# Optimization experiments

Measured on AMD Instinct MI355X. Metric: run time of the kernel, lower is better.

Reference implementation:

```python
import jax, jax.numpy as jnp
import numpy as np

D = 512
H = 8
W = 128  # window_size
HD = D // H
EPS = 1e-5


def _layernorm(x, g, b):
    mu = jnp.mean(x, axis=-1, keepdims=True)
    var = jnp.mean(jnp.square(x - mu), axis=-1, keepdims=True)
    return (x - mu) * jax.lax.rsqrt(var + EPS) * g + b


def setup_inputs() -> dict:
    key = jax.random.key(0)
    ks = jax.random.split(key, 6)
    B, S = 4, 8192
    src = jax.random.normal(ks[0], (B, S, D), jnp.float32)
    sc = 1.0 / np.sqrt(D)
    in_proj_w = jax.random.normal(ks[1], (3 * D, D), jnp.float32) * sc
    in_proj_b = jnp.zeros((3 * D,), jnp.float32)
    out_w = jax.random.normal(ks[2], (D, D), jnp.float32) * sc
    out_b = jnp.zeros((D,), jnp.float32)
    w1 = jax.random.normal(ks[3], (4 * D, D), jnp.float32) * sc
    b1 = jnp.zeros((4 * D,), jnp.float32)
    w2 = jax.random.normal(ks[4], (D, 4 * D), jnp.float32) * (1.0 / np.sqrt(4 * D))
    b2 = jnp.zeros((D,), jnp.float32)
    return {
        'src': src,
        'in_proj_w': in_proj_w, 'in_proj_b': in_proj_b,
        'out_w': out_w, 'out_b': out_b,
        'ln1_g': jnp.ones((D,), jnp.float32), 'ln1_b': jnp.zeros((D,), jnp.float32),
        'w1': w1, 'b1': b1, 'w2': w2, 'b2': b2,
        'ln2_g': jnp.ones((D,), jnp.float32), 'ln2_b': jnp.zeros((D,), jnp.float32),
    }


def reference(src, in_proj_w, in_proj_b, out_w, out_b, ln1_g, ln1_b,
              w1, b1, w2, b2, ln2_g, ln2_b):
    B, S, _ = src.shape
    nW = S // W
    x = src.reshape(B, nW, W, D)  # block-diagonal windows
    # packed qkv projection (torch MultiheadAttention in_proj)
    qkv = jnp.einsum('bnwd,ed->bnwe', x, in_proj_w) + in_proj_b
    q, k, v = jnp.split(qkv, 3, axis=-1)
    q = q.reshape(B, nW, W, H, HD)
    k = k.reshape(B, nW, W, H, HD)
    v = v.reshape(B, nW, W, H, HD)
    scores = jnp.einsum('bnqhd,bnkhd->bnhqk', q, k) / np.sqrt(HD)
    probs = jax.nn.softmax(scores, axis=-1)
    attn = jnp.einsum('bnhqk,bnkhd->bnqhd', probs, v).reshape(B, nW, W, D)
    attn = jnp.einsum('bnwd,ed->bnwe', attn, out_w) + out_b
    x = _layernorm(x + attn, ln1_g, ln1_b)
    ff = jnp.einsum('bnwf,df->bnwd', jax.nn.relu(jnp.einsum('bnwd,fd->bnwf', x, w1) + b1), w2) + b2
    x = _layernorm(x + ff, ln2_g, ln2_b)
    return x.reshape(B, S, D)
```

## Files before the change

### kernel.cpp

```cpp
#include <hip/hip_runtime.h>
#include <hip/hip_bf16.h>
#include <math.h>

typedef __bf16 bf16;
typedef bf16 bf16x8 __attribute__((ext_vector_type(8)));
typedef bf16 bf16x4 __attribute__((ext_vector_type(4)));
typedef float f32x4 __attribute__((ext_vector_type(4)));

#define MFMA16(a, b, c) __builtin_amdgcn_mfma_f32_16x16x32_bf16(a, b, c, 0, 0, 0)

__device__ __forceinline__ uint32_t swz(uint32_t base, uint32_t row, uint32_t rs, uint32_t cb) {
    return base + row * rs + (((cb >> 4) ^ (row & 7u)) << 4) + (cb & 15u);
}

__device__ __forceinline__ void gload16(const void* g, void* l) {
    __builtin_amdgcn_global_load_lds((const __attribute__((address_space(1))) void*)g,
                                     (__attribute__((address_space(3))) void*)l, 16, 0, 0);
}



__global__ void wcvt_kernel(const float* __restrict__ wqkv, const float* __restrict__ wout,
                            const float* __restrict__ w1f, const float* __restrict__ w2f,
                            bf16* __restrict__ o) {
    int i = blockIdx.x * blockDim.x + threadIdx.x;
    const float* s;
    int soff, doff;
    if (i < 98304) {
        int u = i;
        int tile = u >> 11, c = (u >> 9) & 3, nn = u & 511;
        int n = (tile >> 4) * 512 + nn;
        int k = (tile & 15) * 32 + c * 8;
        s = wqkv; soff = n * 512 + k; doff = u * 8;
    } else if (i < 131072) {
        int u = i - 98304;
        int tile = u >> 11, c = (u >> 9) & 3, nn = u & 511;
        int k = tile * 32 + c * 8;
        s = wout; soff = nn * 512 + k; doff = 786432 + u * 8;
    } else if (i < 262144) {
        int u = i - 131072;
        int tile = u >> 11, c = (u >> 9) & 3, nn = u & 511;
        int n = (tile >> 4) * 512 + nn;
        int k = (tile & 15) * 32 + c * 8;
        s = w1f; soff = n * 512 + k; doff = 1048576 + u * 8;
    } else {
        int u = i - 262144;
        int t = u >> 11, c = (u >> 9) & 3, nn = u & 511;
        int k = t * 32 + c * 8;
        s = w2f; soff = nn * 2048 + k; doff = 2097152 + u * 8;
    }
    float4 v0 = *(const float4*)(s + soff);
    float4 v1 = *(const float4*)(s + soff + 4);
    bf16x8 h = { (bf16)v0.x, (bf16)v0.y, (bf16)v0.z, (bf16)v0.w,
                 (bf16)v1.x, (bf16)v1.y, (bf16)v1.z, (bf16)v1.w };
    *(bf16x8*)(o + doff) = h;
}

__global__ void xcvt_kernel(float* __restrict__ src) {
    int row = blockIdx.x * 4 + (threadIdx.x >> 6);
    int l = threadIdx.x & 63;
    float* rp = src + (size_t)row * 512 + l * 8;
    float4 v0 = *(const float4*)rp;
    float4 v1 = *(const float4*)(rp + 4);
    asm volatile("s_waitcnt vmcnt(0)" ::: "memory");
    bf16x8 h = { (bf16)v0.x, (bf16)v0.y, (bf16)v0.z, (bf16)v0.w,
                 (bf16)v1.x, (bf16)v1.y, (bf16)v1.z, (bf16)v1.w };
    *(bf16x8*)((bf16*)(src + (size_t)row * 512) + l * 8) = h;
}

extern "C" __global__ __launch_bounds__(512, 2)
void qkv_kernel(const char* __restrict__ xb, const char* __restrict__ Wqkvp,
                const float* __restrict__ bqkv, char* __restrict__ qOb,
                char* __restrict__ kvb) {
    extern __shared__ char smem[];
    const int tid = threadIdx.x;
    const int w = tid >> 6, lane = tid & 63, l16 = lane & 15, quad = lane >> 4;
    const int wm = w >> 2, wn = w & 3;
    const int mb = blockIdx.x, cb = blockIdx.y;

    f32x4 acc[4][8];
#pragma unroll
    for (int i = 0; i < 4; ++i)
#pragma unroll
        for (int nt = 0; nt < 8; ++nt) acc[i][nt] = (f32x4){0.f, 0.f, 0.f, 0.f};

#define QKV_STAGE(ib, t)                                                               \
    {                                                                                  \
        int ca = w >> 1, rg = w & 1;           \
        gload16(xb + (size_t)(mb * 128 + rg * 64 + lane) * 2048 + (t) * 64 + ca * 16,  \
                smem + (uint32_t)(ib) * 8192u + ca * 2048 + rg * 1024);                \
        _Pragma("unroll")                                                              \
        for (int j = 0; j < 4; ++j) {      \
            int idx = w * 4 + j, c = idx >> 3, ng = idx & 7;                           \
            gload16(Wqkvp + (size_t)(cb * 16 + (t)) * 32768 + c * 8192 + ng * 1024 + lane * 16, \
                    smem + 24576u + (uint32_t)(ib) * 32768u + (uint32_t)c * 8192 + (uint32_t)ng * 1024); \
        }                                                                              \
    }

    QKV_STAGE(0, 0);
    QKV_STAGE(1, 1);
    asm volatile("s_waitcnt vmcnt(5)" ::: "memory");
    __builtin_amdgcn_s_barrier();

    int ib = 0;
#pragma unroll 1
    for (int t = 0; t < 16; ++t) {
        int in2 = ib + 2; if (in2 >= 3) in2 -= 3;
        if (t + 2 < 16) QKV_STAGE(in2, t + 2);
        const uint32_t A0 = (uint32_t)ib * 8192u;
        const uint32_t B0 = 24576u + (uint32_t)ib * 32768u;
        bf16x8 a[4];
#pragma unroll
        for (int i = 0; i < 4; ++i)
            a[i] = *(const bf16x8*)(smem + A0 + quad * 2048 + (wm * 64 + i * 16 + l16) * 16);
#pragma unroll
        for (int nt = 0; nt < 8; ++nt) {
            bf16x8 b = *(const bf16x8*)(smem + B0 + quad * 8192 + (wn * 128 + nt * 16 + l16) * 16);
#pragma unroll
            for (int i = 0; i < 4; ++i) acc[i][nt] = MFMA16(a[i], b, acc[i][nt]);
        }
        if (t + 2 < 16) asm volatile("s_waitcnt vmcnt(5)" ::: "memory");
        else            asm volatile("s_waitcnt vmcnt(0)" ::: "memory");
        __builtin_amdgcn_s_barrier();
        ib = (ib == 2) ? 0 : ib + 1;
    }
#undef QKV_STAGE

    const uint32_t sb = 24576u + (uint32_t)w * 4096u;
#pragma unroll
    for (int i = 0; i < 4; ++i) {
#pragma unroll
        for (int nt = 0; nt < 8; ++nt) {
            float bb = bqkv[cb * 512 + wn * 128 + nt * 16 + l16];
#pragma unroll
            for (int r = 0; r < 4; ++r)
                *(bf16*)(smem + swz(sb, quad * 4 + r, 256, (nt * 16 + l16) * 2)) =
                    (bf16)(acc[i][nt][r] + bb);
        }
        asm volatile("s_waitcnt lgkmcnt(0)" ::: "memory");
#pragma unroll
        for (int j = 0; j < 4; ++j) {
            int uu = j * 64 + lane;
            int row = uu >> 4, ch = uu & 15;
            bf16x8 v = *(bf16x8*)(smem + swz(sb, row, 256, ch * 16));
            size_t row_g = (size_t)(mb * 128 + wm * 64 + i * 16 + row);
            int nb2 = wn * 256 + ch * 16;
            if (cb == 0)      *(bf16x8*)(qOb + row_g * 1024 + nb2) = v;
            else if (cb == 1) *(bf16x8*)(kvb + row_g * 2048 + nb2) = v;
            else              *(bf16x8*)(kvb + row_g * 2048 + 1024 + nb2) = v;
        }
        asm volatile("s_waitcnt lgkmcnt(0)" ::: "memory");
    }
}

#define AVT 0u
#define ASCR 16384u
extern "C" __global__ __launch_bounds__(512, 4)
void attn_kernel(char* __restrict__ qOb, const char* __restrict__ kvb) {
    extern __shared__ char smem[];
    const int tid = threadIdx.x;
    const int wid = tid >> 6, lane = tid & 63, l16 = lane & 15, quad = lane >> 4;
    const int win = blockIdx.x >> 3, head = blockIdx.x & 7;
    const size_t wrow0 = (size_t)win * 128;
    f32x4 zero4 = { 0.f, 0.f, 0.f, 0.f };

    {
        int key = tid >> 2, d0 = (tid & 3) * 16;
        const char* vs = kvb + (wrow0 + key) * 2048 + 1024 + head * 128 + d0 * 2;
#pragma unroll
        for (int j = 0; j < 2; ++j) {
            bf16x8 v = *(const bf16x8*)(vs + j * 16);
#pragma unroll
            for (int e = 0; e < 8; ++e)
                *(bf16*)(smem + swz(AVT, d0 + j * 8 + e, 256, key * 2)) = v[e];
        }
    }
    __syncthreads();

    bf16x8 qf[2];
#pragma unroll
    for (int ks = 0; ks < 2; ++ks)
        qf[ks] = *(const bf16x8*)(qOb + (wrow0 + wid * 16 + l16) * 1024 + head * 128 + ks * 64 + quad * 16);

    f32x4 sa[8];
#pragma unroll
    for (int nt = 0; nt < 8; ++nt) sa[nt] = zero4;
#pragma unroll
    for (int nt = 0; nt < 8; ++nt)
#pragma unroll
        for (int ks = 0; ks < 2; ++ks) {
            bf16x8 kb = *(const bf16x8*)(kvb + (wrow0 + nt * 16 + l16) * 2048 + head * 128 + ks * 64 + quad * 16);
            sa[nt] = MFMA16(qf[ks], kb, sa[nt]);
        }
#pragma unroll
    for (int nt = 0; nt < 8; ++nt) sa[nt] *= 0.125f;
#pragma unroll
    for (int r = 0; r < 4; ++r) {
        float m = sa[0][r];
#pragma unroll
        for (int nt = 1; nt < 8; ++nt) m = fmaxf(m, sa[nt][r]);
#pragma unroll
        for (int sft = 1; sft < 16; sft <<= 1) m = fmaxf(m, __shfl_xor(m, sft, 64));
        float s = 0.f;
#pragma unroll
        for (int nt = 0; nt < 8; ++nt) {
            float e = __expf(sa[nt][r] - m);
            sa[nt][r] = e;
            s += e;
        }
#pragma unroll
        for (int sft = 1; sft < 16; sft <<= 1) s += __shfl_xor(s, sft, 64);
        float inv = 1.0f / s;
#pragma unroll
        for (int nt = 0; nt < 8; ++nt) sa[nt][r] *= inv;
    }

    const uint32_t sb = ASCR + (uint32_t)wid * 2048;
    bf16x8 pf[4];
#pragma unroll
    for (int hf = 0; hf < 2; ++hf) {
#pragma unroll
        for (int nt = 0; nt < 4; ++nt)
#pragma unroll
            for (int r = 0; r < 4; ++r)
                *(bf16*)(smem + swz(sb, quad * 4 + r, 128, (nt * 16 + l16) * 2)) = (bf16)sa[hf * 4 + nt][r];
        asm volatile("s_waitcnt lgkmcnt(0)" ::: "memory");
#pragma unroll
        for (int ks = 0; ks < 2; ++ks)
            pf[hf * 2 + ks] = *(bf16x8*)(smem + swz(sb, l16, 128, ks * 64 + quad * 16));
        asm volatile("s_waitcnt lgkmcnt(0)" ::: "memory");
    }

    f32x4 ov[4];
#pragma unroll
    for (int nt = 0; nt < 4; ++nt) {
        ov[nt] = zero4;
#pragma unroll
        for (int ks = 0; ks < 4; ++ks) {
            bf16x8 vb = *(bf16x8*)(smem + swz(AVT, nt * 16 + l16, 256, ks * 64 + quad * 16));
            ov[nt] = MFMA16(pf[ks], vb, ov[nt]);
        }
    }
#pragma unroll
    for (int hf = 0; hf < 2; ++hf) {
#pragma unroll
        for (int nt = 0; nt < 2; ++nt)
#pragma unroll
            for (int r = 0; r < 4; ++r)
                *(bf16*)(smem + swz(sb, quad * 4 + r, 128, (nt * 16 + l16) * 2)) = (bf16)ov[hf * 2 + nt][r];
        asm volatile("s_waitcnt lgkmcnt(0)" ::: "memory");
        {
            int row = lane >> 2, ch = lane & 3;
            bf16x8 v = *(bf16x8*)(smem + swz(sb, row, 128, ch * 16));
            *(bf16x8*)(qOb + (wrow0 + wid * 16 + row) * 1024 + head * 128 + hf * 64 + ch * 16) = v;
        }
        asm volatile("s_waitcnt lgkmcnt(0)" ::: "memory");
    }
}

extern "C" __global__ __launch_bounds__(512, 2)
void outproj_kernel(char* __restrict__ srcb, const char* __restrict__ qOb,
                    const char* __restrict__ Woutp, const float* __restrict__ bout,
                    const float* __restrict__ g1, const float* __restrict__ be1) {
    extern __shared__ char smem[];
    const int tid = threadIdx.x;
    const int w = tid >> 6, lane = tid & 63, l16 = lane & 15, quad = lane >> 4;
    const int wm = w >> 2, wn = w & 3;
    const int mb = blockIdx.x;

    f32x4 acc[4][8];
#pragma unroll
    for (int i = 0; i < 4; ++i)
#pragma unroll
        for (int nt = 0; nt < 8; ++nt) acc[i][nt] = (f32x4){0.f, 0.f, 0.f, 0.f};

#define OP_STAGE(ib, t)                                                                \
    {                                                                                  \
        int ca = w >> 1, rg = w & 1;           \
        gload16(qOb + (size_t)(mb * 128 + rg * 64 + lane) * 1024 + (t) * 64 + ca * 16, \
                smem + (uint32_t)(ib) * 8192u + ca * 2048 + rg * 1024);                \
        _Pragma("unroll")                                                              \
        for (int j = 0; j < 4; ++j) {      \
            int idx = w * 4 + j, c = idx >> 3, ng = idx & 7;                           \
            gload16(Woutp + (size_t)(t) * 32768 + c * 8192 + ng * 1024 + lane * 16,    \
                    smem + 24576u + (uint32_t)(ib) * 32768u + (uint32_t)c * 8192 + (uint32_t)ng * 1024); \
        }                                                                              \
    }

    OP_STAGE(0, 0);
    OP_STAGE(1, 1);
    asm volatile("s_waitcnt vmcnt(5)" ::: "memory");
    __builtin_amdgcn_s_barrier();

    int ib = 0;
#pragma unroll 1
    for (int t = 0; t < 16; ++t) {
        int in2 = ib + 2; if (in2 >= 3) in2 -= 3;
        if (t + 2 < 16) OP_STAGE(in2, t + 2);
        const uint32_t A0 = (uint32_t)ib * 8192u;
        const uint32_t B0 = 24576u + (uint32_t)ib * 32768u;
        bf16x8 a[4];
#pragma unroll
        for (int i = 0; i < 4; ++i)
            a[i] = *(const bf16x8*)(smem + A0 + quad * 2048 + (wm * 64 + i * 16 + l16) * 16);
#pragma unroll
        for (int nt = 0; nt < 8; ++nt) {
            bf16x8 b = *(const bf16x8*)(smem + B0 + quad * 8192 + (wn * 128 + nt * 16 + l16) * 16);
#pragma unroll
            for (int i = 0; i < 4; ++i) acc[i][nt] = MFMA16(a[i], b, acc[i][nt]);
        }
        if (t + 2 < 16) asm volatile("s_waitcnt vmcnt(5)" ::: "memory");
        else            asm volatile("s_waitcnt vmcnt(0)" ::: "memory");
        __builtin_amdgcn_s_barrier();
        ib = (ib == 2) ? 0 : ib + 1;
    }
#undef OP_STAGE

#pragma unroll
    for (int nt = 0; nt < 8; ++nt) {
        int col = wn * 128 + nt * 16 + l16;
        float bb = bout[col];
#pragma unroll
        for (int i = 0; i < 4; ++i)
#pragma unroll
            for (int r = 0; r < 4; ++r) {
                int row = mb * 128 + wm * 64 + i * 16 + quad * 4 + r;
                float xv = (float)*(const bf16*)(srcb + (size_t)row * 2048 + col * 2);
                acc[i][nt][r] += bb + xv;
            }
    }
    float ps[4][4], ps2[4][4];
#pragma unroll
    for (int i = 0; i < 4; ++i)
#pragma unroll
        for (int r = 0; r < 4; ++r) {
            float s = 0.f, s2 = 0.f;
#pragma unroll
            for (int nt = 0; nt < 8; ++nt) {
                float v = acc[i][nt][r];
                s += v;
                s2 += v * v;
            }
#pragma unroll
            for (int sft = 1; sft < 16; sft <<= 1) {
                s += __shfl_xor(s, sft, 64);
                s2 += __shfl_xor(s2, sft, 64);
            }
            ps[i][r] = s;
            ps2[i][r] = s2;
        }
    if (l16 == 0) {
#pragma unroll
        for (int i = 0; i < 4; ++i)
#pragma unroll
            for (int r = 0; r < 4; ++r) {
                int row_l = wm * 64 + i * 16 + quad * 4 + r;
                *(float*)(smem + row_l * 32 + wn * 8) = ps[i][r];
                *(float*)(smem + row_l * 32 + wn * 8 + 4) = ps2[i][r];
            }
    }
    __syncthreads();
    const uint32_t sb = 24576u + (uint32_t)w * 4096u;
#pragma unroll
    for (int i = 0; i < 4; ++i) {
#pragma unroll
        for (int r = 0; r < 4; ++r) {
            int row_l = wm * 64 + i * 16 + quad * 4 + r;
            float S = 0.f, S2 = 0.f;
#pragma unroll
            for (int w4 = 0; w4 < 4; ++w4) {
                S += *(const float*)(smem + row_l * 32 + w4 * 8);
                S2 += *(const float*)(smem + row_l * 32 + w4 * 8 + 4);
            }
            float mu = S * (1.0f / 512.0f);
            float var = S2 * (1.0f / 512.0f) - mu * mu;
            float rstd = rsqrtf(var + 1e-5f);
#pragma unroll
            for (int nt = 0; nt < 8; ++nt) {
                int col = wn * 128 + nt * 16 + l16;
                float v = (acc[i][nt][r] - mu) * rstd * g1[col] + be1[col];
                *(bf16*)(smem + swz(sb, quad * 4 + r, 256, (nt * 16 + l16) * 2)) = (bf16)v;
            }
        }
        asm volatile("s_waitcnt lgkmcnt(0)" ::: "memory");
#pragma unroll
        for (int j = 0; j < 4; ++j) {
            int uu = j * 64 + lane;
            int row = uu >> 4, ch = uu & 15;
            bf16x8 v = *(bf16x8*)(smem + swz(sb, row, 256, ch * 16));
            *(bf16x8*)(srcb + (size_t)(mb * 128 + wm * 64 + i * 16 + row) * 2048 + 1024 +
                       wn * 256 + ch * 16) = v;
        }
        asm volatile("s_waitcnt lgkmcnt(0)" ::: "memory");
    }
}

extern "C" __global__ __launch_bounds__(512, 2)
void ff1_kernel(char* __restrict__ srcb, const char* __restrict__ W1p,
                const float* __restrict__ b1, char* __restrict__ doutb,
                char* __restrict__ wsOb) {
    extern __shared__ char smem[];
    const int tid = threadIdx.x;
    const int w = tid >> 6, lane = tid & 63, l16 = lane & 15, quad = lane >> 4;
    const int wm = w >> 2, wn = w & 3;
    const int mb = blockIdx.x, cb = blockIdx.y;

    f32x4 acc[4][8];
#pragma unroll
    for (int i = 0; i < 4; ++i)
#pragma unroll
        for (int nt = 0; nt < 8; ++nt) acc[i][nt] = (f32x4){0.f, 0.f, 0.f, 0.f};

#define FF1_STAGE(ib, t)                                                               \
    {                                                                                  \
        int ca = w >> 1, rg = w & 1;             \
        gload16(srcb + (size_t)(mb * 128 + rg * 64 + lane) * 2048 + 1024 + (t) * 64 + ca * 16, \
                smem + (uint32_t)(ib) * 8192u + ca * 2048 + rg * 1024);                \
        _Pragma("unroll")                                                              \
        for (int j = 0; j < 4; ++j) {      \
            int idx = w * 4 + j, c = idx >> 3, ng = idx & 7;                           \
            gload16(W1p + (size_t)(cb * 16 + (t)) * 32768 + c * 8192 + ng * 1024 + lane * 16, \
                    smem + 24576u + (uint32_t)(ib) * 32768u + (uint32_t)c * 8192 + (uint32_t)ng * 1024); \
        }                                                                              \
    }

    FF1_STAGE(0, 0);
    FF1_STAGE(1, 1);
    asm volatile("s_waitcnt vmcnt(5)" ::: "memory");
    __builtin_amdgcn_s_barrier();

    int ib = 0;
#pragma unroll 1
    for (int t = 0; t < 16; ++t) {
        int in2 = ib + 2; if (in2 >= 3) in2 -= 3;
        if (t + 2 < 16) FF1_STAGE(in2, t + 2);
        const uint32_t A0 = (uint32_t)ib * 8192u;
        const uint32_t B0 = 24576u + (uint32_t)ib * 32768u;
        bf16x8 a[4];
#pragma unroll
        for (int i = 0; i < 4; ++i)
            a[i] = *(const bf16x8*)(smem + A0 + quad * 2048 + (wm * 64 + i * 16 + l16) * 16);
#pragma unroll
        for (int nt = 0; nt < 8; ++nt) {
            bf16x8 b = *(const bf16x8*)(smem + B0 + quad * 8192 + (wn * 128 + nt * 16 + l16) * 16);
#pragma unroll
            for (int i = 0; i < 4; ++i) acc[i][nt] = MFMA16(a[i], b, acc[i][nt]);
        }
        if (t + 2 < 16) asm volatile("s_waitcnt vmcnt(5)" ::: "memory");
        else            asm volatile("s_waitcnt vmcnt(0)" ::: "memory");
        __builtin_amdgcn_s_barrier();
        ib = (ib == 2) ? 0 : ib + 1;
    }
#undef FF1_STAGE

    const uint32_t sb = 24576u + (uint32_t)w * 4096u;
#pragma unroll
    for (int i = 0; i < 4; ++i) {
#pragma unroll
        for (int nt = 0; nt < 8; ++nt) {
            float bb = b1[cb * 512 + wn * 128 + nt * 16 + l16];
#pragma unroll
            for (int r = 0; r < 4; ++r)
                *(bf16*)(smem + swz(sb, quad * 4 + r, 256, (nt * 16 + l16) * 2)) =
                    (bf16)fmaxf(acc[i][nt][r] + bb, 0.0f);
        }
        asm volatile("s_waitcnt lgkmcnt(0)" ::: "memory");
#pragma unroll
        for (int j = 0; j < 4; ++j) {
            int uu = j * 64 + lane;
            int row = uu >> 4, ch = uu & 15;
            bf16x8 v = *(bf16x8*)(smem + swz(sb, row, 256, ch * 16));
            size_t row_g = (size_t)(mb * 128 + wm * 64 + i * 16 + row);
            int nb2 = wn * 256 + ch * 16;
            if (cb < 2)       *(bf16x8*)(doutb + row_g * 2048 + cb * 1024 + nb2) = v;
            else if (cb == 2) *(bf16x8*)(srcb + row_g * 2048 + nb2) = v;
            else              *(bf16x8*)(wsOb + row_g * 1024 + nb2) = v;
        }
        asm volatile("s_waitcnt lgkmcnt(0)" ::: "memory");
    }
}

extern "C" __global__ __launch_bounds__(512, 2)
void ff2_kernel(char* __restrict__ doutb, const char* __restrict__ srcb,
                const char* __restrict__ wsOb, const char* __restrict__ W2p,
                const float* __restrict__ b2, const float* __restrict__ g2,
                const float* __restrict__ be2) {
    extern __shared__ char smem[];
    const int tid = threadIdx.x;
    const int w = tid >> 6, lane = tid & 63, l16 = lane & 15, quad = lane >> 4;
    const int wm = w >> 2, wn = w & 3;
    const int mb = blockIdx.x;

    f32x4 acc[4][8];
#pragma unroll
    for (int i = 0; i < 4; ++i)
#pragma unroll
        for (int nt = 0; nt < 8; ++nt) acc[i][nt] = (f32x4){0.f, 0.f, 0.f, 0.f};

#define FF2_STAGE(ib, t)                                                               \
    {                                                                                  \
        const char* hb; int rstride, koffb;                                            \
        if ((t) < 32)      { hb = doutb; rstride = 2048; koffb = (t) * 64; }           \
        else if ((t) < 48) { hb = srcb;  rstride = 2048; koffb = ((t) - 32) * 64; }    \
        else               { hb = wsOb;  rstride = 1024; koffb = ((t) - 48) * 64; }    \
        int ca = w >> 1, rg = w & 1;           \
        gload16(hb + (size_t)(mb * 128 + rg * 64 + lane) * rstride + koffb + ca * 16,  \
                smem + (uint32_t)(ib) * 8192u + ca * 2048 + rg * 1024);                \
        _Pragma("unroll")                                                              \
        for (int j = 0; j < 4; ++j) {      \
            int idx = w * 4 + j, c = idx >> 3, ng = idx & 7;                           \
            gload16(W2p + (size_t)(t) * 32768 + c * 8192 + ng * 1024 + lane * 16,      \
                    smem + 24576u + (uint32_t)(ib) * 32768u + (uint32_t)c * 8192 + (uint32_t)ng * 1024); \
        }                                                                              \
    }

    FF2_STAGE(0, 0);
    FF2_STAGE(1, 1);
    asm volatile("s_waitcnt vmcnt(5)" ::: "memory");
    __builtin_amdgcn_s_barrier();

    int ib = 0;
#pragma unroll 1
    for (int t = 0; t < 64; ++t) {
        int in2 = ib + 2; if (in2 >= 3) in2 -= 3;
        if (t + 2 < 64) FF2_STAGE(in2, t + 2);
        const uint32_t A0 = (uint32_t)ib * 8192u;
        const uint32_t B0 = 24576u + (uint32_t)ib * 32768u;
        bf16x8 a[4];
#pragma unroll
        for (int i = 0; i < 4; ++i)
            a[i] = *(const bf16x8*)(smem + A0 + quad * 2048 + (wm * 64 + i * 16 + l16) * 16);
#pragma unroll
        for (int nt = 0; nt < 8; ++nt) {
            bf16x8 b = *(const bf16x8*)(smem + B0 + quad * 8192 + (wn * 128 + nt * 16 + l16) * 16);
#pragma unroll
            for (int i = 0; i < 4; ++i) acc[i][nt] = MFMA16(a[i], b, acc[i][nt]);
        }
        if (t + 2 < 64) asm volatile("s_waitcnt vmcnt(5)" ::: "memory");
        else            asm volatile("s_waitcnt vmcnt(0)" ::: "memory");
        __builtin_amdgcn_s_barrier();
        ib = (ib == 2) ? 0 : ib + 1;
    }
#undef FF2_STAGE

#pragma unroll
    for (int nt = 0; nt < 8; ++nt) {
        int col = wn * 128 + nt * 16 + l16;
        float bb = b2[col];
#pragma unroll
        for (int i = 0; i < 4; ++i)
#pragma unroll
            for (int r = 0; r < 4; ++r) {
                int row = mb * 128 + wm * 64 + i * 16 + quad * 4 + r;
                float x1v = (float)*(const bf16*)(srcb + (size_t)row * 2048 + 1024 + col * 2);
                acc[i][nt][r] += bb + x1v;
            }
    }
    float ps[4][4], ps2[4][4];
#pragma unroll
    for (int i = 0; i < 4; ++i)
#pragma unroll
        for (int r = 0; r < 4; ++r) {
            float s = 0.f, s2 = 0.f;
#pragma unroll
            for (int nt = 0; nt < 8; ++nt) {
                float v = acc[i][nt][r];
                s += v;
                s2 += v * v;
            }
#pragma unroll
            for (int sft = 1; sft < 16; sft <<= 1) {
                s += __shfl_xor(s, sft, 64);
                s2 += __shfl_xor(s2, sft, 64);
            }
            ps[i][r] = s;
            ps2[i][r] = s2;
        }
    if (l16 == 0) {
#pragma unroll
        for (int i = 0; i < 4; ++i)
#pragma unroll
            for (int r = 0; r < 4; ++r) {
                int row_l = wm * 64 + i * 16 + quad * 4 + r;
                *(float*)(smem + row_l * 32 + wn * 8) = ps[i][r];
                *(float*)(smem + row_l * 32 + wn * 8 + 4) = ps2[i][r];
            }
    }
    __syncthreads();
#pragma unroll
    for (int i = 0; i < 4; ++i)
#pragma unroll
        for (int r = 0; r < 4; ++r) {
            int row_l = wm * 64 + i * 16 + quad * 4 + r;
            float S = 0.f, S2 = 0.f;
#pragma unroll
            for (int w4 = 0; w4 < 4; ++w4) {
                S += *(const float*)(smem + row_l * 32 + w4 * 8);
                S2 += *(const float*)(smem + row_l * 32 + w4 * 8 + 4);
            }
            float mu = S * (1.0f / 512.0f);
            float var = S2 * (1.0f / 512.0f) - mu * mu;
            float rstd = rsqrtf(var + 1e-5f);
            size_t row = (size_t)(mb * 128 + row_l);
#pragma unroll
            for (int nt = 0; nt < 8; ++nt) {
                int col = wn * 128 + nt * 16 + l16;
                *(float*)(doutb + row * 2048 + col * 4) =
                    (acc[i][nt][r] - mu) * rstd * g2[col] + be2[col];
            }
        }
}

extern "C" void kernel_launch(void* const* d_in, const int* in_sizes, int n_in,
                              void* d_out, int out_size, void* d_ws, size_t ws_size,
                              hipStream_t stream) {
    (void)in_sizes; (void)n_in; (void)out_size; (void)ws_size;
    float* src = (float*)d_in[0];
    const float* ipw = (const float*)d_in[1];
    const float* ipb = (const float*)d_in[2];
    const float* ow  = (const float*)d_in[3];
    const float* ob  = (const float*)d_in[4];
    const float* g1  = (const float*)d_in[5];
    const float* be1 = (const float*)d_in[6];
    const float* w1  = (const float*)d_in[7];
    const float* b1  = (const float*)d_in[8];
    const float* w2  = (const float*)d_in[9];
    const float* b2  = (const float*)d_in[10];
    const float* g2  = (const float*)d_in[11];
    const float* be2 = (const float*)d_in[12];
    bf16* ws = (bf16*)d_ws;
    char* srcb = (char*)src;
    char* doutb = (char*)d_out;
    char* qOb = (char*)d_ws + 6291456;

    wcvt_kernel<<<1536, 256, 0, stream>>>(ipw, ow, w1, w2, ws);
    xcvt_kernel<<<8192, 256, 0, stream>>>(src);

    hipFuncSetAttribute((const void*)qkv_kernel, hipFuncAttributeMaxDynamicSharedMemorySize, 122880);
    hipFuncSetAttribute((const void*)attn_kernel, hipFuncAttributeMaxDynamicSharedMemorySize, 32768);
    hipFuncSetAttribute((const void*)outproj_kernel, hipFuncAttributeMaxDynamicSharedMemorySize, 122880);
    hipFuncSetAttribute((const void*)ff1_kernel, hipFuncAttributeMaxDynamicSharedMemorySize, 122880);
    hipFuncSetAttribute((const void*)ff2_kernel, hipFuncAttributeMaxDynamicSharedMemorySize, 122880);

    qkv_kernel<<<dim3(256, 3), 512, 122880, stream>>>(srcb, (const char*)ws, ipb, qOb, doutb);
    attn_kernel<<<2048, 512, 32768, stream>>>(qOb, doutb);
    outproj_kernel<<<256, 512, 122880, stream>>>(srcb, qOb, (const char*)(ws + 786432), ob, g1, be1);
    ff1_kernel<<<dim3(256, 4), 512, 122880, stream>>>(srcb, (const char*)(ws + 1048576), b1, doutb, qOb);
    ff2_kernel<<<256, 512, 122880, stream>>>(doutb, srcb, qOb, (const char*)(ws + 2097152), b2, g2, be2);
}
```

Measured before the change: 497.3 us.

## Split GEMM k-loop into two phases interleaving loads with prioritized MFMA bursts

Restructures the main loop of all four GEMM kernels into two phases. Each phase reads a batch of LDS fragments, issues part of the next stage's global-to-LDS loads, synchronizes, then runs an MFMA burst at raised wave priority (s_setprio) behind a sched_barrier. The goal is to interleave memory issue with matrix work and keep the MFMA pipe fed across waves. The cost is extra barriers per k-step and holding 8 B fragments in registers, which adds pressure under launch_bounds(512,2).

Result: no change. 505.5 us (+1.7%).

```diff
diff --git a/kernel.cpp b/kernel.cpp
--- a/kernel.cpp
+++ b/kernel.cpp
@@ -68,6 +68,52 @@
     *(bf16x8*)((bf16*)(src + (size_t)row * 512) + l * 8) = h;
 }
 
+#define PHASED_LOOP(NT)                                                                \
+    int ib = 0;                                                                        \
+    _Pragma("unroll 1")                                                                \
+    for (int t = 0; t < (NT); ++t) {                                                   \
+        int in2 = ib + 2; if (in2 >= 3) in2 -= 3;                                      \
+        const uint32_t A0 = (uint32_t)ib * 8192u;                                      \
+        const uint32_t B0 = 24576u + (uint32_t)ib * 32768u;                            \
+        bf16x8 a[4], b[8];                                                             \
+                                                                \
+        _Pragma("unroll")                                                              \
+        for (int i = 0; i < 4; ++i)                                                    \
+            a[i] = *(const bf16x8*)(smem + A0 + quad * 2048 + (wm * 64 + i * 16 + l16) * 16); \
+        _Pragma("unroll")                                                              \
+        for (int nt = 0; nt < 4; ++nt)                                                 \
+            b[nt] = *(const bf16x8*)(smem + B0 + quad * 8192 + (wn * 128 + nt * 16 + l16) * 16); \
+        if (t + 2 < (NT)) { STAGE_A(in2, t + 2); STAGE_B(in2, t + 2, 0); }             \
+        __builtin_amdgcn_s_barrier();                                                  \
+        asm volatile("s_waitcnt lgkmcnt(0)" ::: "memory");                             \
+        __builtin_amdgcn_sched_barrier(0);                                             \
+        __builtin_amdgcn_s_setprio(1);                                                 \
+        _Pragma("unroll")                                                              \
+        for (int nt = 0; nt < 4; ++nt)                                                 \
+            _Pragma("unroll")                                                          \
+            for (int i = 0; i < 4; ++i) acc[i][nt] = MFMA16(a[i], b[nt], acc[i][nt]);  \
+        __builtin_amdgcn_s_setprio(0);                                                 \
+        __builtin_amdgcn_s_barrier();                                                  \
+                                                                \
+        _Pragma("unroll")                                                              \
+        for (int nt = 4; nt < 8; ++nt)                                                 \
+            b[nt] = *(const bf16x8*)(smem + B0 + quad * 8192 + (wn * 128 + nt * 16 + l16) * 16); \
+        if (t + 2 < (NT)) { STAGE_B(in2, t + 2, 1); STAGE_B(in2, t + 2, 2); STAGE_B(in2, t + 2, 3); } \
+        __builtin_amdgcn_s_barrier();                                                  \
+        asm volatile("s_waitcnt lgkmcnt(0)" ::: "memory");                             \
+        __builtin_amdgcn_sched_barrier(0);                                             \
+        __builtin_amdgcn_s_setprio(1);                                                 \
+        _Pragma("unroll")                                                              \
+        for (int nt = 4; nt < 8; ++nt)                                                 \
+            _Pragma("unroll")                                                          \
+            for (int i = 0; i < 4; ++i) acc[i][nt] = MFMA16(a[i], b[nt], acc[i][nt]);  \
+        __builtin_amdgcn_s_setprio(0);                                                 \
+        if (t + 2 < (NT)) asm volatile("s_waitcnt vmcnt(5)" ::: "memory");             \
+        else              asm volatile("s_waitcnt vmcnt(0)" ::: "memory");             \
+        __builtin_amdgcn_s_barrier();                                                  \
+        ib = (ib == 2) ? 0 : ib + 1;                                                   \
+    }
+
 extern "C" __global__ __launch_bounds__(512, 2)
 void qkv_kernel(const char* __restrict__ xb, const char* __restrict__ Wqkvp,
                 const float* __restrict__ bqkv, char* __restrict__ qOb,
@@ -84,47 +130,27 @@
 #pragma unroll
         for (int nt = 0; nt < 8; ++nt) acc[i][nt] = (f32x4){0.f, 0.f, 0.f, 0.f};
 
-#define QKV_STAGE(ib, t)                                                               \
-    {                                                                                  \
-        int ca = w >> 1, rg = w & 1;           \
-        gload16(xb + (size_t)(mb * 128 + rg * 64 + lane) * 2048 + (t) * 64 + ca * 16,  \
-                smem + (uint32_t)(ib) * 8192u + ca * 2048 + rg * 1024);                \
-        _Pragma("unroll")                                                              \
-        for (int j = 0; j < 4; ++j) {      \
-            int idx = w * 4 + j, c = idx >> 3, ng = idx & 7;                           \
-            gload16(Wqkvp + (size_t)(cb * 16 + (t)) * 32768 + c * 8192 + ng * 1024 + lane * 16, \
-                    smem + 24576u + (uint32_t)(ib) * 32768u + (uint32_t)c * 8192 + (uint32_t)ng * 1024); \
-        }                                                                              \
-    }
-
-    QKV_STAGE(0, 0);
-    QKV_STAGE(1, 1);
+#define STAGE_A(ib_, t_)                                                               \
+    {                                                                                  \
+        int ca = w >> 1, rg = w & 1;                                                   \
+        gload16(xb + (size_t)(mb * 128 + rg * 64 + lane) * 2048 + (t_) * 64 + ca * 16, \
+                smem + (uint32_t)(ib_) * 8192u + ca * 2048 + rg * 1024);               \
+    }
+#define STAGE_B(ib_, t_, j_)                                                           \
+    {                                                                                  \
+        int idx = w * 4 + (j_), c = idx >> 3, ng = idx & 7;                            \
+        gload16(Wqkvp + (size_t)(cb * 16 + (t_)) * 32768 + c * 8192 + ng * 1024 + lane * 16, \
+                smem + 24576u + (uint32_t)(ib_) * 32768u + (uint32_t)c * 8192 + (uint32_t)ng * 1024); \
+    }
+
+    STAGE_A(0, 0); STAGE_B(0, 0, 0); STAGE_B(0, 0, 1); STAGE_B(0, 0, 2); STAGE_B(0, 0, 3);
+    STAGE_A(1, 1); STAGE_B(1, 1, 0); STAGE_B(1, 1, 1); STAGE_B(1, 1, 2); STAGE_B(1, 1, 3);
     asm volatile("s_waitcnt vmcnt(5)" ::: "memory");
     __builtin_amdgcn_s_barrier();
 
-    int ib = 0;
-#pragma unroll 1
-    for (int t = 0; t < 16; ++t) {
-        int in2 = ib + 2; if (in2 >= 3) in2 -= 3;
-        if (t + 2 < 16) QKV_STAGE(in2, t + 2);
-        const uint32_t A0 = (uint32_t)ib * 8192u;
-        const uint32_t B0 = 24576u + (uint32_t)ib * 32768u;
-        bf16x8 a[4];
-#pragma unroll
-        for (int i = 0; i < 4; ++i)
-            a[i] = *(const bf16x8*)(smem + A0 + quad * 2048 + (wm * 64 + i * 16 + l16) * 16);
-#pragma unroll
-        for (int nt = 0; nt < 8; ++nt) {
-            bf16x8 b = *(const bf16x8*)(smem + B0 + quad * 8192 + (wn * 128 + nt * 16 + l16) * 16);
-#pragma unroll
-            for (int i = 0; i < 4; ++i) acc[i][nt] = MFMA16(a[i], b, acc[i][nt]);
-        }
-        if (t + 2 < 16) asm volatile("s_waitcnt vmcnt(5)" ::: "memory");
-        else            asm volatile("s_waitcnt vmcnt(0)" ::: "memory");
-        __builtin_amdgcn_s_barrier();
-        ib = (ib == 2) ? 0 : ib + 1;
-    }
-#undef QKV_STAGE
+    PHASED_LOOP(16)
+#undef STAGE_A
+#undef STAGE_B
 
     const uint32_t sb = 24576u + (uint32_t)w * 4096u;
 #pragma unroll
@@ -274,47 +300,27 @@
 #pragma unroll
         for (int nt = 0; nt < 8; ++nt) acc[i][nt] = (f32x4){0.f, 0.f, 0.f, 0.f};
 
-#define OP_STAGE(ib, t)                                                                \
-    {                                                                                  \
-        int ca = w >> 1, rg = w & 1;           \
-        gload16(qOb + (size_t)(mb * 128 + rg * 64 + lane) * 1024 + (t) * 64 + ca * 16, \
-                smem + (uint32_t)(ib) * 8192u + ca * 2048 + rg * 1024);                \
-        _Pragma("unroll")                                                              \
-        for (int j = 0; j < 4; ++j) {      \
-            int idx = w * 4 + j, c = idx >> 3, ng = idx & 7;                           \
-            gload16(Woutp + (size_t)(t) * 32768 + c * 8192 + ng * 1024 + lane * 16,    \
-                    smem + 24576u + (uint32_t)(ib) * 32768u + (uint32_t)c * 8192 + (uint32_t)ng * 1024); \
-        }                                                                              \
-    }
-
-    OP_STAGE(0, 0);
-    OP_STAGE(1, 1);
+#define STAGE_A(ib_, t_)                                                               \
+    {                                                                                  \
+        int ca = w >> 1, rg = w & 1;                                                   \
+        gload16(qOb + (size_t)(mb * 128 + rg * 64 + lane) * 1024 + (t_) * 64 + ca * 16, \
+                smem + (uint32_t)(ib_) * 8192u + ca * 2048 + rg * 1024);               \
+    }
+#define STAGE_B(ib_, t_, j_)                                                           \
+    {                                                                                  \
+        int idx = w * 4 + (j_), c = idx >> 3, ng = idx & 7;                            \
+        gload16(Woutp + (size_t)(t_) * 32768 + c * 8192 + ng * 1024 + lane * 16,       \
+                smem + 24576u + (uint32_t)(ib_) * 32768u + (uint32_t)c * 8192 + (uint32_t)ng * 1024); \
+    }
+
+    STAGE_A(0, 0); STAGE_B(0, 0, 0); STAGE_B(0, 0, 1); STAGE_B(0, 0, 2); STAGE_B(0, 0, 3);
+    STAGE_A(1, 1); STAGE_B(1, 1, 0); STAGE_B(1, 1, 1); STAGE_B(1, 1, 2); STAGE_B(1, 1, 3);
     asm volatile("s_waitcnt vmcnt(5)" ::: "memory");
     __builtin_amdgcn_s_barrier();
 
-    int ib = 0;
-#pragma unroll 1
-    for (int t = 0; t < 16; ++t) {
-        int in2 = ib + 2; if (in2 >= 3) in2 -= 3;
-        if (t + 2 < 16) OP_STAGE(in2, t + 2);
-        const uint32_t A0 = (uint32_t)ib * 8192u;
-        const uint32_t B0 = 24576u + (uint32_t)ib * 32768u;
-        bf16x8 a[4];
-#pragma unroll
-        for (int i = 0; i < 4; ++i)
-            a[i] = *(const bf16x8*)(smem + A0 + quad * 2048 + (wm * 64 + i * 16 + l16) * 16);
-#pragma unroll
-        for (int nt = 0; nt < 8; ++nt) {
-            bf16x8 b = *(const bf16x8*)(smem + B0 + quad * 8192 + (wn * 128 + nt * 16 + l16) * 16);
-#pragma unroll
-            for (int i = 0; i < 4; ++i) acc[i][nt] = MFMA16(a[i], b, acc[i][nt]);
-        }
-        if (t + 2 < 16) asm volatile("s_waitcnt vmcnt(5)" ::: "memory");
-        else            asm volatile("s_waitcnt vmcnt(0)" ::: "memory");
-        __builtin_amdgcn_s_barrier();
-        ib = (ib == 2) ? 0 : ib + 1;
-    }
-#undef OP_STAGE
+    PHASED_LOOP(16)
+#undef STAGE_A
+#undef STAGE_B
 
 #pragma unroll
     for (int nt = 0; nt < 8; ++nt) {
@@ -411,47 +417,27 @@
 #pragma unroll
         for (int nt = 0; nt < 8; ++nt) acc[i][nt] = (f32x4){0.f, 0.f, 0.f, 0.f};
 
-#define FF1_STAGE(ib, t)                                                               \
-    {                                                                                  \
-        int ca = w >> 1, rg = w & 1;             \
-        gload16(srcb + (size_t)(mb * 128 + rg * 64 + lane) * 2048 + 1024 + (t) * 64 + ca * 16, \
-                smem + (uint32_t)(ib) * 8192u + ca * 2048 + rg * 1024);                \
-        _Pragma("unroll")                                                              \
-        for (int j = 0; j < 4; ++j) {      \
-            int idx = w * 4 + j, c = idx >> 3, ng = idx & 7;                           \
-            gload16(W1p + (size_t)(cb * 16 + (t)) * 32768 + c * 8192 + ng * 1024 + lane * 16, \
-                    smem + 24576u + (uint32_t)(ib) * 32768u + (uint32_t)c * 8192 + (uint32_t)ng * 1024); \
-        }                                                                              \
-    }
-
-    FF1_STAGE(0, 0);
-    FF1_STAGE(1, 1);
+#define STAGE_A(ib_, t_)                                                               \
+    {                                                                                  \
+        int ca = w >> 1, rg = w & 1;                                                   \
+        gload16(srcb + (size_t)(mb * 128 + rg * 64 + lane) * 2048 + 1024 + (t_) * 64 + ca * 16, \
+                smem + (uint32_t)(ib_) * 8192u + ca * 2048 + rg * 1024);               \
+    }
+#define STAGE_B(ib_, t_, j_)                                                           \
+    {                                                                                  \
+        int idx = w * 4 + (j_), c = idx >> 3, ng = idx & 7;                            \
+        gload16(W1p + (size_t)(cb * 16 + (t_)) * 32768 + c * 8192 + ng * 1024 + lane * 16, \
+                smem + 24576u + (uint32_t)(ib_) * 32768u + (uint32_t)c * 8192 + (uint32_t)ng * 1024); \
+    }
+
+    STAGE_A(0, 0); STAGE_B(0, 0, 0); STAGE_B(0, 0, 1); STAGE_B(0, 0, 2); STAGE_B(0, 0, 3);
+    STAGE_A(1, 1); STAGE_B(1, 1, 0); STAGE_B(1, 1, 1); STAGE_B(1, 1, 2); STAGE_B(1, 1, 3);
     asm volatile("s_waitcnt vmcnt(5)" ::: "memory");
     __builtin_amdgcn_s_barrier();
 
-    int ib = 0;
-#pragma unroll 1
-    for (int t = 0; t < 16; ++t) {
-        int in2 = ib + 2; if (in2 >= 3) in2 -= 3;
-        if (t + 2 < 16) FF1_STAGE(in2, t + 2);
-        const uint32_t A0 = (uint32_t)ib * 8192u;
-        const uint32_t B0 = 24576u + (uint32_t)ib * 32768u;
-        bf16x8 a[4];
-#pragma unroll
-        for (int i = 0; i < 4; ++i)
-            a[i] = *(const bf16x8*)(smem + A0 + quad * 2048 + (wm * 64 + i * 16 + l16) * 16);
-#pragma unroll
-        for (int nt = 0; nt < 8; ++nt) {
-            bf16x8 b = *(const bf16x8*)(smem + B0 + quad * 8192 + (wn * 128 + nt * 16 + l16) * 16);
-#pragma unroll
-            for (int i = 0; i < 4; ++i) acc[i][nt] = MFMA16(a[i], b, acc[i][nt]);
-        }
-        if (t + 2 < 16) asm volatile("s_waitcnt vmcnt(5)" ::: "memory");
-        else            asm volatile("s_waitcnt vmcnt(0)" ::: "memory");
-        __builtin_amdgcn_s_barrier();
-        ib = (ib == 2) ? 0 : ib + 1;
-    }
-#undef FF1_STAGE
+    PHASED_LOOP(16)
+#undef STAGE_A
+#undef STAGE_B
 
     const uint32_t sb = 24576u + (uint32_t)w * 4096u;
 #pragma unroll
@@ -497,51 +483,31 @@
 #pragma unroll
         for (int nt = 0; nt < 8; ++nt) acc[i][nt] = (f32x4){0.f, 0.f, 0.f, 0.f};
 
-#define FF2_STAGE(ib, t)                                                               \
+#define STAGE_A(ib_, t_)                                                               \
     {                                                                                  \
         const char* hb; int rstride, koffb;                                            \
-        if ((t) < 32)      { hb = doutb; rstride = 2048; koffb = (t) * 64; }           \
-        else if ((t) < 48) { hb = srcb;  rstride = 2048; koffb = ((t) - 32) * 64; }    \
-        else               { hb = wsOb;  rstride = 1024; koffb = ((t) - 48) * 64; }    \
-        int ca = w >> 1, rg = w & 1;           \
+        if ((t_) < 32)      { hb = doutb; rstride = 2048; koffb = (t_) * 64; }         \
+        else if ((t_) < 48) { hb = srcb;  rstride = 2048; koffb = ((t_) - 32) * 64; }  \
+        else                { hb = wsOb;  rstride = 1024; koffb = ((t_) - 48) * 64; }  \
+        int ca = w >> 1, rg = w & 1;                                                   \
         gload16(hb + (size_t)(mb * 128 + rg * 64 + lane) * rstride + koffb + ca * 16,  \
-                smem + (uint32_t)(ib) * 8192u + ca * 2048 + rg * 1024);                \
-        _Pragma("unroll")                                                              \
-        for (int j = 0; j < 4; ++j) {      \
-            int idx = w * 4 + j, c = idx >> 3, ng = idx & 7;                           \
-            gload16(W2p + (size_t)(t) * 32768 + c * 8192 + ng * 1024 + lane * 16,      \
-                    smem + 24576u + (uint32_t)(ib) * 32768u + (uint32_t)c * 8192 + (uint32_t)ng * 1024); \
-        }                                                                              \
-    }
-
-    FF2_STAGE(0, 0);
-    FF2_STAGE(1, 1);
+                smem + (uint32_t)(ib_) * 8192u + ca * 2048 + rg * 1024);               \
+    }
+#define STAGE_B(ib_, t_, j_)                                                           \
+    {                                                                                  \
+        int idx = w * 4 + (j_), c = idx >> 3, ng = idx & 7;                            \
+        gload16(W2p + (size_t)(t_) * 32768 + c * 8192 + ng * 1024 + lane * 16,         \
+                smem + 24576u + (uint32_t)(ib_) * 32768u + (uint32_t)c * 8192 + (uint32_t)ng * 1024); \
+    }
+
+    STAGE_A(0, 0); STAGE_B(0, 0, 0); STAGE_B(0, 0, 1); STAGE_B(0, 0, 2); STAGE_B(0, 0, 3);
+    STAGE_A(1, 1); STAGE_B(1, 1, 0); STAGE_B(1, 1, 1); STAGE_B(1, 1, 2); STAGE_B(1, 1, 3);
     asm volatile("s_waitcnt vmcnt(5)" ::: "memory");
     __builtin_amdgcn_s_barrier();
 
-    int ib = 0;
-#pragma unroll 1
-    for (int t = 0; t < 64; ++t) {
-        int in2 = ib + 2; if (in2 >= 3) in2 -= 3;
-        if (t + 2 < 64) FF2_STAGE(in2, t + 2);
-        const uint32_t A0 = (uint32_t)ib * 8192u;
-        const uint32_t B0 = 24576u + (uint32_t)ib * 32768u;
-        bf16x8 a[4];
-#pragma unroll
-        for (int i = 0; i < 4; ++i)
-            a[i] = *(const bf16x8*)(smem + A0 + quad * 2048 + (wm * 64 + i * 16 + l16) * 16);
-#pragma unroll
-        for (int nt = 0; nt < 8; ++nt) {
-            bf16x8 b = *(const bf16x8*)(smem + B0 + quad * 8192 + (wn * 128 + nt * 16 + l16) * 16);
-#pragma unroll
-            for (int i = 0; i < 4; ++i) acc[i][nt] = MFMA16(a[i], b, acc[i][nt]);
-        }
-        if (t + 2 < 64) asm volatile("s_waitcnt vmcnt(5)" ::: "memory");
-        else            asm volatile("s_waitcnt vmcnt(0)" ::: "memory");
-        __builtin_amdgcn_s_barrier();
-        ib = (ib == 2) ? 0 : ib + 1;
-    }
-#undef FF2_STAGE
+    PHASED_LOOP(64)
+#undef STAGE_A
+#undef STAGE_B
 
 #pragma unroll
     for (int nt = 0; nt < 8; ++nt) {
```
